# Optimization experiments

Measured on AMD Instinct MI355X. Metric: run time of the kernel, lower is better.

The kernel has to match this reference:

```python
import jax, jax.numpy as jnp
import numpy as np

B, H, W = 8, 64, 64
DIM, DIM_OUT, HEADS = 448, 896, 16
WIN, STRIDE = 14, 2
MLP_DIM = int(DIM_OUT * 4.0)
EPS = 1e-6
HD = DIM_OUT // HEADS
SCALE = HD ** -0.5


def _ln(x, g, b):
    m = jnp.mean(x, -1, keepdims=True)
    v = jnp.var(x, -1, keepdims=True)
    return (x - m) * jax.lax.rsqrt(v + EPS) * g + b


def _maxpool(x, s):
    # Keras MaxPool2D(pool_size=s, strides=s, padding='valid'), NHWC
    return jax.lax.reduce_window(x, -jnp.inf, jax.lax.max, (1, s, s, 1), (1, s, s, 1), 'VALID')


def setup_inputs() -> dict:
    key = jax.random.key(0)
    ks = jax.random.split(key, 8)
    rn = lambda k, shape: (jax.random.normal(k, shape, jnp.float32) * 0.02)
    return {
        "x": jax.random.normal(ks[0], (B, H, W, DIM), jnp.float32),
        "ln1_g": jnp.ones((DIM,), jnp.float32), "ln1_b": jnp.zeros((DIM,), jnp.float32),
        "qkv_w": rn(ks[1], (DIM, 3 * DIM_OUT)), "qkv_b": jnp.zeros((3 * DIM_OUT,), jnp.float32),
        "attn_proj_w": rn(ks[2], (DIM_OUT, DIM_OUT)), "attn_proj_b": jnp.zeros((DIM_OUT,), jnp.float32),
        "skip_w": rn(ks[3], (DIM, DIM_OUT)), "skip_b": jnp.zeros((DIM_OUT,), jnp.float32),
        "ln2_g": jnp.ones((DIM_OUT,), jnp.float32), "ln2_b": jnp.zeros((DIM_OUT,), jnp.float32),
        "mlp1_w": rn(ks[4], (DIM_OUT, MLP_DIM)), "mlp1_b": jnp.zeros((MLP_DIM,), jnp.float32),
        "mlp2_w": rn(ks[5], (MLP_DIM, DIM_OUT)), "mlp2_b": jnp.zeros((DIM_OUT,), jnp.float32),
    }


def reference(x, ln1_g, ln1_b, qkv_w, qkv_b, attn_proj_w, attn_proj_b,
              skip_w, skip_b, ln2_g, ln2_b, mlp1_w, mlp1_b, mlp2_w, mlp2_b):
    hn = _ln(x, ln1_g, ln1_b)                              # [B,H,W,DIM]
    # dim != dim_out: residual = proj(layernormed); then residual max-pooled
    shortcut = _maxpool(hn @ skip_w + skip_b, STRIDE)      # [B,H/2,W/2,DIM_OUT]

    # window partition (pad 64 -> 70, 5x5 windows of 14x14)
    pad_h = (WIN - H % WIN) % WIN
    pad_w = (WIN - W % WIN) % WIN
    hp = jnp.pad(hn, ((0, 0), (0, pad_h), (0, pad_w), (0, 0)))
    Hp, Wp = H + pad_h, W + pad_w
    nh, nw = Hp // WIN, Wp // WIN
    win = hp.reshape(B, nh, WIN, nw, WIN, DIM).transpose(0, 1, 3, 2, 4, 5)
    win = win.reshape(B * nh * nw, WIN, WIN, DIM)          # [Bw,14,14,DIM]

    # multi-scale attention with query pooling
    Bw = B * nh * nw
    qkv = (win @ qkv_w + qkv_b).reshape(Bw, WIN * WIN, 3, HEADS, HD)
    q, k, v = qkv[:, :, 0], qkv[:, :, 1], qkv[:, :, 2]
    q = _maxpool(q.reshape(Bw, WIN, WIN, DIM_OUT), STRIDE)  # [Bw,7,7,DIM_OUT]
    WQ = WIN // STRIDE
    q = q.reshape(Bw, WQ * WQ, HEADS, HD)
    attn = jax.nn.softmax(jnp.einsum('bqhd,bkhd->bhqk', q * SCALE, k), axis=-1)
    out = jnp.einsum('bhqk,bkhd->bqhd', attn, v).reshape(Bw, WQ, WQ, DIM_OUT)
    out = out @ attn_proj_w + attn_proj_b                  # [Bw,7,7,DIM_OUT]

    # window unpartition at pooled resolution (window 7, padded 35 -> crop 32)
    H2, W2 = H // STRIDE, W // STRIDE
    win2 = WIN // STRIDE
    Hp2 = H2 + (win2 - H2 % win2) % win2
    Wp2 = W2 + (win2 - W2 % win2) % win2
    xo = out.reshape(B, nh, nw, win2, win2, DIM_OUT).transpose(0, 1, 3, 2, 4, 5)
    xo = xo.reshape(B, Hp2, Wp2, DIM_OUT)[:, :H2, :W2, :]

    y = shortcut + xo
    hn2 = _ln(y, ln2_g, ln2_b)
    mlp = jax.nn.gelu(hn2 @ mlp1_w + mlp1_b, approximate=False) @ mlp2_w + mlp2_b
    return y + mlp
```

## Files before the change

### kernel.cpp

```cpp
#include <hip/hip_runtime.h>
#include <hip/hip_bf16.h>

typedef unsigned short u16;
typedef __bf16 bf16x8 __attribute__((ext_vector_type(8)));
typedef float f32x4 __attribute__((ext_vector_type(4)));

__device__ __forceinline__ float bf2f(u16 u) {
    unsigned v = ((unsigned)u) << 16;
    return __builtin_bit_cast(float, v);
}
__device__ __forceinline__ u16 f2bf(float f) {
    unsigned x = __builtin_bit_cast(unsigned, f);
    unsigned r = x + (0x7fffu + ((x >> 16) & 1u));
    return (u16)(r >> 16);
}
__device__ __forceinline__ void gload16(const void* g, void* l) {
    __builtin_amdgcn_global_load_lds(
        (const __attribute__((address_space(1))) void*)g,
        (__attribute__((address_space(3))) void*)l, 16, 0, 0);
}

__global__ __launch_bounds__(256) void transpose_w(const float* __restrict__ src,
    u16* __restrict__ dst, int K, int N)
{
    __shared__ u16 T[64][33];
    int k0 = blockIdx.x * 32, n0 = blockIdx.y * 64;
    int t = threadIdx.x;
    int nc = t & 63, krb = (t >> 6) * 8;
#pragma unroll
    for (int j = 0; j < 8; j++) {
        int kr = krb + j;
        T[nc][kr] = f2bf(src[(size_t)(k0 + kr) * N + n0 + nc]);
    }
    __syncthreads();
    int r = t >> 2, c0 = (t & 3) * 8;
    u16 tmp[8];
#pragma unroll
    for (int i = 0; i < 8; i++) tmp[i] = T[r][c0 + i];
    *(uint4*)&dst[(size_t)(n0 + r) * K + k0 + c0] = *(uint4*)tmp;
}

__global__ void zfill(u16* p) { p[threadIdx.x] = 0; }

template<int C>
__global__ __launch_bounds__(256) void ln_kernel(const float* __restrict__ xf,
    const float* __restrict__ g, const float* __restrict__ b,
    u16* __restrict__ out, int npix)
{
    int wid = threadIdx.x >> 6, lane = threadIdx.x & 63;
    int pix = blockIdx.x * 4 + wid;
    if (pix >= npix) return;
    constexpr int J = C / 64;
    float v[J];
    float s = 0.f, s2 = 0.f;
#pragma unroll
    for (int j = 0; j < J; j++) {
        int c = lane + j * 64;
        float t = xf[(size_t)pix * C + c];
        v[j] = t; s += t; s2 += t * t;
    }
#pragma unroll
    for (int off = 32; off; off >>= 1) {
        s  += __shfl_xor(s,  off, 64);
        s2 += __shfl_xor(s2, off, 64);
    }
    float mean = s / C;
    float var = fmaxf(s2 / C - mean * mean, 0.f);
    float rs = rsqrtf(var + 1e-6f);
#pragma unroll
    for (int j = 0; j < J; j++) {
        int c = lane + j * 64;
        float o = (v[j] - mean) * rs * g[c] + b[c];
        out[(size_t)pix * C + c] = f2bf(o);
    }
}

enum { GA_NONE = 0, GA_WIN = 1 };
enum { EPI_STORE = 0, EPI_GELU = 1, EPI_PROJ = 2, EPI_OUT = 3, EPI_QKV = 4,
       EPI_POOL = 5 };

template<int BM, int GATHER, int EPI, int SWZ>
__global__ __launch_bounds__(256, (BM == 64) ? 6 : 4) void gemm_t(
    const u16* __restrict__ A, const u16* __restrict__ BT,
    const u16* __restrict__ zrow, const float* __restrict__ bias,
    u16* __restrict__ Cb, u16* __restrict__ Cb2,
    float* __restrict__ Yf, float* __restrict__ Of,
    int M, int N, int K, int nbn)
{
    constexpr int MI = BM / 32;
    constexpr int PA = BM / 64;
    constexpr int ASZ = BM * 32, BSZ = 128 * 32;
    __shared__ __align__(16) u16 As[2][ASZ];
    __shared__ __align__(16) u16 Bs[2][BSZ];
    __shared__ int rowsrc[BM];

    const int tid = threadIdx.x;
    int bm, bn;
    if (SWZ) {
        int nwg = gridDim.x, orig = blockIdx.x;
        int q = nwg >> 3, r = nwg & 7;
        int xcd = orig & 7, idx = orig >> 3;
        int wg = (xcd < r ? xcd * (q + 1) : r * (q + 1) + (xcd - r) * q) + idx;
        bm = wg / nbn; bn = wg - bm * nbn;
    } else {
        bm = blockIdx.x; bn = blockIdx.y;
    }

    if (GATHER == GA_WIN) {
        if (tid < BM) {
            int gm = bm * BM + tid;
            int src = -1;
            if (gm < M) {
                int w = gm / 196, t = gm % 196;
                int b = w / 25, wh = (w / 5) % 5, ww = w % 5;
                int ty = t / 14, tx = t % 14;
                int gh = wh * 14 + ty, gw = ww * 14 + tx;
                if (gh < 64 && gw < 64) src = (b * 64 + gh) * 64 + gw;
            }
            rowsrc[tid] = src;
        }
        __syncthreads();
    }

    const int wid = tid >> 6, lane = tid & 63;
    const int wm = wid >> 1, wn = wid & 1;
    const int frow = lane & 15, quad = lane >> 4;

    const int srow = tid >> 2, schunk = tid & 3;
    const int ssw = schunk ^ ((srow ^ (srow >> 2)) & 3);

    const u16* gA[PA]; int stA[PA];
#pragma unroll
    for (int p = 0; p < PA; p++) {
        int r = srow + p * 64;
        int src;
        if (GATHER == GA_WIN) {
            src = rowsrc[r];
        } else {
            int gm = bm * BM + r;
            src = (gm < M) ? gm : -1;
        }
        gA[p]  = (src >= 0) ? A + (size_t)src * K + ssw * 8 : zrow + ssw * 8;
        stA[p] = (src >= 0) ? 32 : 0;
    }
    const u16* gB[2];
#pragma unroll
    for (int p = 0; p < 2; p++)
        gB[p] = BT + (size_t)(bn * 128 + srow + p * 64) * K + ssw * 8;

    const int csw = quad ^ ((frow ^ (frow >> 2)) & 3);
    int offA[MI], offB[4];
#pragma unroll
    for (int mi = 0; mi < MI; mi++)
        offA[mi] = (wm * (BM / 2) + mi * 16 + frow) * 32 + csw * 8;
#pragma unroll
    for (int ni = 0; ni < 4; ni++)
        offB[ni] = (wn * 64 + ni * 16 + frow) * 32 + csw * 8;

    f32x4 acc[MI][4] = {};

    auto stageAdv = [&](int buf) {
#pragma unroll
        for (int p = 0; p < PA; p++) {
            gload16(gA[p], &As[buf][tid * 8 + p * 2048]);
            gA[p] += stA[p];
        }
#pragma unroll
        for (int p = 0; p < 2; p++) {
            gload16(gB[p], &Bs[buf][tid * 8 + p * 2048]);
            gB[p] += 32;
        }
    };
    auto wait_loads = [&]() {
        if constexpr (PA == 2) asm volatile("s_waitcnt vmcnt(4)" ::: "memory");
        else                   asm volatile("s_waitcnt vmcnt(3)" ::: "memory");
    };

    stageAdv(0);
    stageAdv(1);
    wait_loads();
    __builtin_amdgcn_s_barrier();

    int cur = 0;
    const int NK = K / 32;
    for (int kt = 0; kt < NK; kt++) {
        bf16x8 af[MI], bfr[4];
#pragma unroll
        for (int mi = 0; mi < MI; mi++)
            af[mi] = *(const bf16x8*)&As[cur][offA[mi]];
#pragma unroll
        for (int ni = 0; ni < 4; ni++)
            bfr[ni] = *(const bf16x8*)&Bs[cur][offB[ni]];
        asm volatile("s_waitcnt lgkmcnt(0)" ::: "memory");
        __builtin_amdgcn_s_barrier();
        if (kt + 2 < NK) stageAdv(cur);

#pragma unroll
        for (int mi = 0; mi < MI; mi++)
#pragma unroll
            for (int ni = 0; ni < 4; ni++)
                acc[mi][ni] = __builtin_amdgcn_mfma_f32_16x16x32_bf16(
                    af[mi], bfr[ni], acc[mi][ni], 0, 0, 0);

        if (kt + 1 < NK) {
            if (kt + 2 < NK) wait_loads();
            else asm volatile("s_waitcnt vmcnt(0)" ::: "memory");
            __builtin_amdgcn_s_barrier();
        }
        cur ^= 1;
    }

    if (EPI == EPI_POOL) {
        __syncthreads();
        float* Pool = (float*)As;
        if (wm == 1) {
#pragma unroll
            for (int mi = 0; mi < MI; mi++)
#pragma unroll
            for (int ni = 0; ni < 4; ni++) {
                int ox0 = mi * 8 + quad * 2;
                int gnl = wn * 64 + ni * 16 + frow;
                Pool[(ox0 + 0) * 128 + gnl] = fmaxf(acc[mi][ni][0], acc[mi][ni][1]);
                Pool[(ox0 + 1) * 128 + gnl] = fmaxf(acc[mi][ni][2], acc[mi][ni][3]);
            }
        }
        __syncthreads();
        if (wm == 0) {
            int b = bm >> 5, oy = bm & 31;
#pragma unroll
            for (int mi = 0; mi < MI; mi++)
#pragma unroll
            for (int ni = 0; ni < 4; ni++) {
                int ox0 = mi * 8 + quad * 2;
                int gnl = wn * 64 + ni * 16 + frow;
                int gn = bn * 128 + gnl;
                float bv = bias[gn];
                float v0 = fmaxf(fmaxf(acc[mi][ni][0], acc[mi][ni][1]),
                                 Pool[(ox0 + 0) * 128 + gnl]) + bv;
                float v1 = fmaxf(fmaxf(acc[mi][ni][2], acc[mi][ni][3]),
                                 Pool[(ox0 + 1) * 128 + gnl]) + bv;
                size_t pix = (size_t)((b * 32 + oy) * 32 + ox0);
                Yf[pix * 896 + gn] = v0;
                Yf[(pix + 1) * 896 + gn] = v1;
            }
        }
        return;
    }

#pragma unroll
    for (int mi = 0; mi < MI; mi++)
#pragma unroll
    for (int ni = 0; ni < 4; ni++)
#pragma unroll
    for (int i = 0; i < 4; i++) {
        int gm = bm * BM + wm * (BM / 2) + mi * 16 + quad * 4 + i;
        int gn = bn * 128 + wn * 64 + ni * 16 + frow;
        if (gm >= M) continue;
        float val = acc[mi][ni][i] + bias[gn];
        if (EPI == EPI_STORE) {
            Cb[(size_t)gm * N + gn] = f2bf(val);
        } else if (EPI == EPI_QKV) {
            int third = gn / 896;
            int col = gn - third * 896;
            u16* dst = third ? Cb2 : Cb;
            dst[(size_t)gm * 896 + col] = f2bf(val);
        } else if (EPI == EPI_GELU) {
            float ge = 0.5f * val * (1.0f + erff(val * 0.70710678118654752f));
            Cb[(size_t)gm * N + gn] = f2bf(ge);
        } else if (EPI == EPI_PROJ) {
            int w = gm / 49, q = gm % 49;
            int b = w / 25, wh = (w / 5) % 5, ww = w % 5;
            int qy = q / 7, qx = q % 7;
            int oy = wh * 7 + qy, ox = ww * 7 + qx;
            if (oy < 32 && ox < 32) {
                size_t pix = (size_t)((b * 32 + oy) * 32 + ox);
                Yf[pix * 896 + gn] += val;
            }
        } else {
            Of[(size_t)gm * 896 + gn] = val + Yf[(size_t)gm * 896 + gn];
        }
    }
}

__global__ __launch_bounds__(256) void qpool(const u16* __restrict__ qf,
                                             u16* __restrict__ qp, int total8)
{
    int id = blockIdx.x * 256 + threadIdx.x;
    if (id >= total8) return;
    int c8 = id % 112, rq = id / 112;
    int c = c8 * 8;
    int q = rq % 49, w = rq / 49;
    int qy = q / 7, qx = q % 7;
    int t0 = (2 * qy) * 14 + 2 * qx;
    const u16* base = qf + (size_t)(w * 196 + t0) * 896 + c;
    uint4 a = *(const uint4*)base;
    uint4 b = *(const uint4*)(base + 896);
    uint4 cc = *(const uint4*)(base + 14 * 896);
    uint4 d = *(const uint4*)(base + 15 * 896);
    u16 ua[8], ub[8], uc[8], ud[8], uo[8];
    *(uint4*)ua = a; *(uint4*)ub = b; *(uint4*)uc = cc; *(uint4*)ud = d;
#pragma unroll
    for (int i = 0; i < 8; i++) {
        float m = fmaxf(fmaxf(bf2f(ua[i]), bf2f(ub[i])),
                        fmaxf(bf2f(uc[i]), bf2f(ud[i])));
        uo[i] = f2bf(m);
    }
    *(uint4*)&qp[(size_t)rq * 896 + c] = *(uint4*)uo;
}

__global__ __launch_bounds__(256) void attn_mfma(const u16* __restrict__ qp,
    const u16* __restrict__ kbuf, const u16* __restrict__ vbuf,
    u16* __restrict__ ao)
{
    __shared__ __align__(16) u16 Ps[64][232];
    __shared__ __align__(16) u16 KV[208 * 72];

    const float SCALE = 0.13363062095621219f;
    const int w = blockIdx.x >> 4, h = blockIdx.x & 15;
    const int tid = threadIdx.x;
    const int wid = tid >> 6, lane = tid & 63;
    const int n16 = lane & 15, quad = lane >> 4;

    for (int idx = tid; idx < 64 * 232 / 8; idx += 256)
        *(uint4*)&Ps[0][idx * 8] = make_uint4(0u, 0u, 0u, 0u);
    for (int idx = tid; idx < 208 * 9; idx += 256) {
        int n = idx / 9, kc = (idx % 9) * 8;
        uint4 val = make_uint4(0u, 0u, 0u, 0u);
        if (n < 196 && kc < 56)
            val = *(const uint4*)(kbuf + (size_t)(w * 196 + n) * 896 + h * 56 + kc);
        *(uint4*)&KV[n * 72 + kc] = val;
    }
    bf16x8 qf[2];
    {
        int m = 16 * wid + n16;
        int row = w * 49 + (m < 49 ? m : 48);
        const u16* src = qp + (size_t)row * 896 + h * 56;
#pragma unroll
        for (int ks = 0; ks < 2; ks++) {
            int kk = ks * 32 + quad * 8;
            uint4 v = make_uint4(0u, 0u, 0u, 0u);
            if (kk < 56) v = *(const uint4*)(src + kk);
            qf[ks] = __builtin_bit_cast(bf16x8, v);
        }
    }
    __syncthreads();

    f32x4 S[13] = {};
#pragma unroll
    for (int nt = 0; nt < 13; nt++) {
#pragma unroll
        for (int ks = 0; ks < 2; ks++) {
            bf16x8 bf = *(const bf16x8*)&KV[(nt * 16 + n16) * 72 + ks * 32 + quad * 8];
            S[nt] = __builtin_amdgcn_mfma_f32_16x16x32_bf16(qf[ks], bf, S[nt], 0, 0, 0);
        }
    }
#pragma unroll
    for (int i = 0; i < 4; i++) {
        float mx = -3.0e38f;
#pragma unroll
        for (int nt = 0; nt < 13; nt++) {
            float v = S[nt][i] * SCALE;
            S[nt][i] = v;
            if (nt < 12 || n16 < 4) mx = fmaxf(mx, v);
        }
        mx = fmaxf(mx, __shfl_xor(mx, 1, 64));
        mx = fmaxf(mx, __shfl_xor(mx, 2, 64));
        mx = fmaxf(mx, __shfl_xor(mx, 4, 64));
        mx = fmaxf(mx, __shfl_xor(mx, 8, 64));
        float sm = 0.f;
#pragma unroll
        for (int nt = 0; nt < 13; nt++) {
            float e = (nt < 12 || n16 < 4) ? __expf(S[nt][i] - mx) : 0.f;
            S[nt][i] = e;
            sm += e;
        }
        sm += __shfl_xor(sm, 1, 64);
        sm += __shfl_xor(sm, 2, 64);
        sm += __shfl_xor(sm, 4, 64);
        sm += __shfl_xor(sm, 8, 64);
        float inv = 1.f / sm;
#pragma unroll
        for (int nt = 0; nt < 13; nt++) S[nt][i] *= inv;
    }
    __syncthreads();

#pragma unroll
    for (int nt = 0; nt < 13; nt++)
#pragma unroll
        for (int i = 0; i < 4; i++)
            Ps[16 * wid + 4 * quad + i][16 * nt + n16] = f2bf(S[nt][i]);

    u16 (*Vs)[232] = reinterpret_cast<u16(*)[232]>(KV);
    for (int idx = tid; idx < 98 * 7; idx += 256) {
        int j2 = idx / 7, dc = idx % 7;
        int j = 2 * j2;
        const u16* vp = vbuf + (size_t)(w * 196 + j) * 896 + h * 56 + dc * 8;
        uint4 a = *(const uint4*)vp;
        uint4 b = *(const uint4*)(vp + 896);
        u16 ua[8], ub[8];
        *(uint4*)ua = a; *(uint4*)ub = b;
#pragma unroll
        for (int i = 0; i < 8; i++) {
            unsigned pair = (unsigned)ua[i] | ((unsigned)ub[i] << 16);
            *(unsigned*)&Vs[dc * 8 + i][j] = pair;
        }
    }
    for (int idx = tid; idx < 64 * 14; idx += 256) {
        int d = idx / 14, c = idx % 14;
        *(unsigned*)&Vs[d][196 + 2 * c] = 0u;
    }
    __syncthreads();

    f32x4 O[4] = {};
#pragma unroll
    for (int ks = 0; ks < 7; ks++) {
        bf16x8 a = *(const bf16x8*)&Ps[16 * wid + n16][ks * 32 + quad * 8];
#pragma unroll
        for (int nt = 0; nt < 4; nt++) {
            bf16x8 b = *(const bf16x8*)&Vs[16 * nt + n16][ks * 32 + quad * 8];
            O[nt] = __builtin_amdgcn_mfma_f32_16x16x32_bf16(a, b, O[nt], 0, 0, 0);
        }
    }
#pragma unroll
    for (int nt = 0; nt < 4; nt++)
#pragma unroll
        for (int i = 0; i < 4; i++) {
            int m = 16 * wid + 4 * quad + i;
            int d = 16 * nt + n16;
            if (m < 49 && d < 56)
                ao[(size_t)(w * 49 + m) * 896 + h * 56 + d] = f2bf(O[nt][i]);
        }
}

extern "C" void kernel_launch(void* const* d_in, const int* in_sizes, int n_in,
                              void* d_out, int out_size, void* d_ws, size_t ws_size,
                              hipStream_t stream)
{
    const float* x    = (const float*)d_in[0];
    const float* ln1g = (const float*)d_in[1];
    const float* ln1b = (const float*)d_in[2];
    const float* qkvw = (const float*)d_in[3];
    const float* qkvb = (const float*)d_in[4];
    const float* pw   = (const float*)d_in[5];
    const float* pb   = (const float*)d_in[6];
    const float* sw   = (const float*)d_in[7];
    const float* sb   = (const float*)d_in[8];
    const float* ln2g = (const float*)d_in[9];
    const float* ln2b = (const float*)d_in[10];
    const float* m1w  = (const float*)d_in[11];
    const float* m1b  = (const float*)d_in[12];
    const float* m2w  = (const float*)d_in[13];
    const float* m2b  = (const float*)d_in[14];

    char* ws = (char*)d_ws;
    u16*   slot1 = (u16*)(ws + 0);
    u16*   vbuf  = (u16*)(ws + 70246400);
    u16*   hn    = (u16*)(ws + 140492800);
    float* Yf    = (float*)(ws + 169852928);
    u16*   qp    = (u16*)(ws + 199213056);
    u16*   ao    = (u16*)(ws + 216774656);
    u16*   swT   = (u16*)(ws + 234336256);
    u16*   qkvT  = (u16*)(ws + 235139072);
    u16*   pwT   = (u16*)(ws + 237547520);
    u16*   zrow  = (u16*)(ws + 239153152);
    u16*   qfull = slot1;
    u16*   kbuf  = slot1;
    u16*   m1    = slot1;
    u16*   hn2   = hn;
    u16*   m1wT  = vbuf;
    u16*   m2wT  = (u16*)(ws + 70246400 + 6422528);
    float* outf  = (float*)d_out;

    zfill<<<1, 128, 0, stream>>>(zrow);
    transpose_w<<<dim3(14, 14), 256, 0, stream>>>(sw,   swT,  448, 896);
    transpose_w<<<dim3(14, 42), 256, 0, stream>>>(qkvw, qkvT, 448, 2688);
    transpose_w<<<dim3(28, 14), 256, 0, stream>>>(pw,   pwT,  896, 896);
    ln_kernel<448><<<8192, 256, 0, stream>>>(x, ln1g, ln1b, hn, 32768);
    gemm_t<128, GA_NONE, EPI_POOL, 1><<<256 * 7, 256, 0, stream>>>(
        hn, swT, zrow, sb, nullptr, nullptr, Yf, nullptr, 32768, 896, 448, 7);
    gemm_t<128, GA_WIN, EPI_STORE, 1><<<307 * 7, 256, 0, stream>>>(
        hn, qkvT, zrow, qkvb, qfull, nullptr, nullptr, nullptr, 39200, 896, 448, 7);
    qpool<<<4288, 256, 0, stream>>>(qfull, qp, 9800 * 112);
    gemm_t<128, GA_WIN, EPI_QKV, 1><<<307 * 14, 256, 0, stream>>>(
        hn, qkvT + (size_t)896 * 448, zrow, qkvb + 896, kbuf, vbuf, nullptr, nullptr,
        39200, 1792, 448, 14);
    attn_mfma<<<3200, 256, 0, stream>>>(qp, kbuf, vbuf, ao);
    transpose_w<<<dim3(28, 56),  256, 0, stream>>>(m1w, m1wT, 896, 3584);
    transpose_w<<<dim3(112, 14), 256, 0, stream>>>(m2w, m2wT, 3584, 896);
    gemm_t<64, GA_NONE, EPI_PROJ, 1><<<154 * 7, 256, 0, stream>>>(
        ao, pwT, zrow, pb, nullptr, nullptr, Yf, nullptr, 9800, 896, 896, 7);
    ln_kernel<896><<<2048, 256, 0, stream>>>(Yf, ln2g, ln2b, hn2, 8192);
    gemm_t<128, GA_NONE, EPI_GELU, 0><<<dim3(64, 28), 256, 0, stream>>>(
        hn2, m1wT, zrow, m1b, m1, nullptr, nullptr, nullptr, 8192, 3584, 896, 28);
    gemm_t<64, GA_NONE, EPI_OUT, 0><<<dim3(128, 7), 256, 0, stream>>>(
        m1, m2wT, zrow, m2b, nullptr, nullptr, Yf, outf, 8192, 896, 3584, 7);
}
```

Measured before the change: 699.1 us.

## Compute QKV on unpadded image and fuse query max-pool into GEMM epilogue

The windowed QKV GEMMs with gather over padded 39200 rows are replaced by one GEMM over the 32768 real pixels producing K and V in image layout, with Q max-pooled in the epilogue and scattered to window order. Padded positions are served by the bias (converted to bf16) in the attention loader and by a separate fill kernel for pooled Q. This removes padded-row compute, the full-resolution Q write/read, and the separate qpool kernel. In exchange attention loads gain per-element address arithmetic and branching.

```diff
diff --git a/kernel.cpp b/kernel.cpp
--- a/kernel.cpp
+++ b/kernel.cpp
@@ -41,6 +41,30 @@
 }
 
 __global__ void zfill(u16* p) { p[threadIdx.x] = 0; }
+
+__global__ __launch_bounds__(256) void cvt_bias(const float* __restrict__ s,
+                                                u16* __restrict__ d, int n)
+{
+    int i = blockIdx.x * 256 + threadIdx.x;
+    if (i < n) d[i] = f2bf(s[i]);
+}
+
+__global__ __launch_bounds__(256) void qfill(const float* __restrict__ qkvb,
+                                             u16* __restrict__ qp)
+{
+    int id = blockIdx.x * 256 + threadIdx.x;
+    if (id >= 9800 * 112) return;
+    int c8 = id % 112, rq = id / 112;
+    int q = rq % 49, w = rq / 49;
+    int qy = q / 7, qx = q - 7 * qy;
+    int wh = (w / 5) % 5, ww = w % 5;
+    if (!((wh == 4 && qy >= 4) || (ww == 4 && qx >= 4))) return;
+    int c = c8 * 8;
+    u16 o[8];
+#pragma unroll
+    for (int i = 0; i < 8; i++) o[i] = f2bf(qkvb[c + i]);
+    *(uint4*)&qp[(size_t)rq * 896 + c] = *(uint4*)o;
+}
 
 template<int C>
 __global__ __launch_bounds__(256) void ln_kernel(const float* __restrict__ xf,
@@ -75,15 +99,14 @@
     }
 }
 
-enum { GA_NONE = 0, GA_WIN = 1 };
-enum { EPI_STORE = 0, EPI_GELU = 1, EPI_PROJ = 2, EPI_OUT = 3, EPI_QKV = 4,
+enum { EPI_STORE = 0, EPI_GELU = 1, EPI_PROJ = 2, EPI_OUT = 3, EPI_QKV3 = 4,
        EPI_POOL = 5 };
 
-template<int BM, int GATHER, int EPI, int SWZ>
+template<int BM, int EPI, int SWZ>
 __global__ __launch_bounds__(256, (BM == 64) ? 6 : 4) void gemm_t(
     const u16* __restrict__ A, const u16* __restrict__ BT,
     const u16* __restrict__ zrow, const float* __restrict__ bias,
-    u16* __restrict__ Cb, u16* __restrict__ Cb2,
+    u16* __restrict__ Cb, u16* __restrict__ Cb2, u16* __restrict__ Cb3,
     float* __restrict__ Yf, float* __restrict__ Of,
     int M, int N, int K, int nbn)
 {
@@ -92,7 +115,6 @@
     constexpr int ASZ = BM * 32, BSZ = 128 * 32;
     __shared__ __align__(16) u16 As[2][ASZ];
     __shared__ __align__(16) u16 Bs[2][BSZ];
-    __shared__ int rowsrc[BM];
 
     const int tid = threadIdx.x;
     int bm, bn;
@@ -106,22 +128,6 @@
         bm = blockIdx.x; bn = blockIdx.y;
     }
 
-    if (GATHER == GA_WIN) {
-        if (tid < BM) {
-            int gm = bm * BM + tid;
-            int src = -1;
-            if (gm < M) {
-                int w = gm / 196, t = gm % 196;
-                int b = w / 25, wh = (w / 5) % 5, ww = w % 5;
-                int ty = t / 14, tx = t % 14;
-                int gh = wh * 14 + ty, gw = ww * 14 + tx;
-                if (gh < 64 && gw < 64) src = (b * 64 + gh) * 64 + gw;
-            }
-            rowsrc[tid] = src;
-        }
-        __syncthreads();
-    }
-
     const int wid = tid >> 6, lane = tid & 63;
     const int wm = wid >> 1, wn = wid & 1;
     const int frow = lane & 15, quad = lane >> 4;
@@ -132,14 +138,8 @@
     const u16* gA[PA]; int stA[PA];
 #pragma unroll
     for (int p = 0; p < PA; p++) {
-        int r = srow + p * 64;
-        int src;
-        if (GATHER == GA_WIN) {
-            src = rowsrc[r];
-        } else {
-            int gm = bm * BM + r;
-            src = (gm < M) ? gm : -1;
-        }
+        int gm = bm * BM + srow + p * 64;
+        int src = (gm < M) ? gm : -1;
         gA[p]  = (src >= 0) ? A + (size_t)src * K + ssw * 8 : zrow + ssw * 8;
         stA[p] = (src >= 0) ? 32 : 0;
     }
@@ -210,7 +210,8 @@
         cur ^= 1;
     }
 
-    if (EPI == EPI_POOL) {
+    const bool qpool_path = (EPI == EPI_QKV3 && bn < 7) || EPI == EPI_POOL;
+    if (qpool_path) {
         __syncthreads();
         float* Pool = (float*)As;
         if (wm == 1) {
@@ -227,6 +228,7 @@
         __syncthreads();
         if (wm == 0) {
             int b = bm >> 5, oy = bm & 31;
+            int wh = oy / 7, qy = oy - 7 * wh;
 #pragma unroll
             for (int mi = 0; mi < MI; mi++)
 #pragma unroll
@@ -239,9 +241,19 @@
                                  Pool[(ox0 + 0) * 128 + gnl]) + bv;
                 float v1 = fmaxf(fmaxf(acc[mi][ni][2], acc[mi][ni][3]),
                                  Pool[(ox0 + 1) * 128 + gnl]) + bv;
-                size_t pix = (size_t)((b * 32 + oy) * 32 + ox0);
-                Yf[pix * 896 + gn] = v0;
-                Yf[(pix + 1) * 896 + gn] = v1;
+                if (EPI == EPI_POOL) {
+                    size_t pix = (size_t)((b * 32 + oy) * 32 + ox0);
+                    Yf[pix * 896 + gn] = v0;
+                    Yf[(pix + 1) * 896 + gn] = v1;
+                } else {
+                    int ox1 = ox0 + 1;
+                    int ww0 = ox0 / 7, qx0 = ox0 - 7 * ww0;
+                    int ww1 = ox1 / 7, qx1 = ox1 - 7 * ww1;
+                    int w0 = b * 25 + wh * 5 + ww0;
+                    int w1 = b * 25 + wh * 5 + ww1;
+                    Cb3[(size_t)(w0 * 49 + qy * 7 + qx0) * 896 + gn] = f2bf(v0);
+                    Cb3[(size_t)(w1 * 49 + qy * 7 + qx1) * 896 + gn] = f2bf(v1);
+                }
             }
         }
         return;
@@ -259,10 +271,10 @@
         float val = acc[mi][ni][i] + bias[gn];
         if (EPI == EPI_STORE) {
             Cb[(size_t)gm * N + gn] = f2bf(val);
-        } else if (EPI == EPI_QKV) {
+        } else if (EPI == EPI_QKV3) {
             int third = gn / 896;
             int col = gn - third * 896;
-            u16* dst = third ? Cb2 : Cb;
+            u16* dst = (third == 1) ? Cb : Cb2;
             dst[(size_t)gm * 896 + col] = f2bf(val);
         } else if (EPI == EPI_GELU) {
             float ge = 0.5f * val * (1.0f + erff(val * 0.70710678118654752f));
@@ -282,35 +294,9 @@
     }
 }
 
-__global__ __launch_bounds__(256) void qpool(const u16* __restrict__ qf,
-                                             u16* __restrict__ qp, int total8)
-{
-    int id = blockIdx.x * 256 + threadIdx.x;
-    if (id >= total8) return;
-    int c8 = id % 112, rq = id / 112;
-    int c = c8 * 8;
-    int q = rq % 49, w = rq / 49;
-    int qy = q / 7, qx = q % 7;
-    int t0 = (2 * qy) * 14 + 2 * qx;
-    const u16* base = qf + (size_t)(w * 196 + t0) * 896 + c;
-    uint4 a = *(const uint4*)base;
-    uint4 b = *(const uint4*)(base + 896);
-    uint4 cc = *(const uint4*)(base + 14 * 896);
-    uint4 d = *(const uint4*)(base + 15 * 896);
-    u16 ua[8], ub[8], uc[8], ud[8], uo[8];
-    *(uint4*)ua = a; *(uint4*)ub = b; *(uint4*)uc = cc; *(uint4*)ud = d;
-#pragma unroll
-    for (int i = 0; i < 8; i++) {
-        float m = fmaxf(fmaxf(bf2f(ua[i]), bf2f(ub[i])),
-                        fmaxf(bf2f(uc[i]), bf2f(ud[i])));
-        uo[i] = f2bf(m);
-    }
-    *(uint4*)&qp[(size_t)rq * 896 + c] = *(uint4*)uo;
-}
-
 __global__ __launch_bounds__(256) void attn_mfma(const u16* __restrict__ qp,
-    const u16* __restrict__ kbuf, const u16* __restrict__ vbuf,
-    u16* __restrict__ ao)
+    const u16* __restrict__ kimg, const u16* __restrict__ vimg,
+    const u16* __restrict__ qkvbf, u16* __restrict__ ao)
 {
     __shared__ __align__(16) u16 Ps[64][232];
     __shared__ __align__(16) u16 KV[208 * 72];
@@ -321,13 +307,22 @@
     const int wid = tid >> 6, lane = tid & 63;
     const int n16 = lane & 15, quad = lane >> 4;
 
+    const int b = w / 25, wh = (w / 5) % 5, ww = w % 5;
+    const int ghb = wh * 14, gwb = ww * 14;
+
     for (int idx = tid; idx < 64 * 232 / 8; idx += 256)
         *(uint4*)&Ps[0][idx * 8] = make_uint4(0u, 0u, 0u, 0u);
     for (int idx = tid; idx < 208 * 9; idx += 256) {
         int n = idx / 9, kc = (idx % 9) * 8;
         uint4 val = make_uint4(0u, 0u, 0u, 0u);
-        if (n < 196 && kc < 56)
-            val = *(const uint4*)(kbuf + (size_t)(w * 196 + n) * 896 + h * 56 + kc);
+        if (n < 196 && kc < 56) {
+            int ty = n / 14, tx = n - 14 * ty;
+            int gh = ghb + ty, gw = gwb + tx;
+            const u16* src = (gh < 64 && gw < 64)
+                ? kimg + (size_t)((b * 64 + gh) * 64 + gw) * 896 + h * 56 + kc
+                : qkvbf + 896 + h * 56 + kc;
+            val = *(const uint4*)src;
+        }
         *(uint4*)&KV[n * 72 + kc] = val;
     }
     bf16x8 qf[2];
@@ -394,11 +389,19 @@
     for (int idx = tid; idx < 98 * 7; idx += 256) {
         int j2 = idx / 7, dc = idx % 7;
         int j = 2 * j2;
-        const u16* vp = vbuf + (size_t)(w * 196 + j) * 896 + h * 56 + dc * 8;
-        uint4 a = *(const uint4*)vp;
-        uint4 b = *(const uint4*)(vp + 896);
+        int ty = j / 14, tx = j - 14 * ty;
+        int gh = ghb + ty, gw = gwb + tx;
+        int off = h * 56 + dc * 8;
+        const u16* p0 = (gh < 64 && gw < 64)
+            ? vimg + (size_t)((b * 64 + gh) * 64 + gw) * 896 + off
+            : qkvbf + 1792 + off;
+        const u16* p1 = (gh < 64 && gw + 1 < 64)
+            ? vimg + (size_t)((b * 64 + gh) * 64 + gw + 1) * 896 + off
+            : qkvbf + 1792 + off;
+        uint4 a = *(const uint4*)p0;
+        uint4 bb = *(const uint4*)p1;
         u16 ua[8], ub[8];
-        *(uint4*)ua = a; *(uint4*)ub = b;
+        *(uint4*)ua = a; *(uint4*)ub = bb;
 #pragma unroll
         for (int i = 0; i < 8; i++) {
             unsigned pair = (unsigned)ua[i] | ((unsigned)ub[i] << 16);
@@ -417,8 +420,8 @@
         bf16x8 a = *(const bf16x8*)&Ps[16 * wid + n16][ks * 32 + quad * 8];
 #pragma unroll
         for (int nt = 0; nt < 4; nt++) {
-            bf16x8 b = *(const bf16x8*)&Vs[16 * nt + n16][ks * 32 + quad * 8];
-            O[nt] = __builtin_amdgcn_mfma_f32_16x16x32_bf16(a, b, O[nt], 0, 0, 0);
+            bf16x8 b2 = *(const bf16x8*)&Vs[16 * nt + n16][ks * 32 + quad * 8];
+            O[nt] = __builtin_amdgcn_mfma_f32_16x16x32_bf16(a, b2, O[nt], 0, 0, 0);
         }
     }
 #pragma unroll
@@ -453,45 +456,47 @@
     const float* m2b  = (const float*)d_in[14];
 
     char* ws = (char*)d_ws;
-    u16*   slot1 = (u16*)(ws + 0);
-    u16*   vbuf  = (u16*)(ws + 70246400);
-    u16*   hn    = (u16*)(ws + 140492800);
-    float* Yf    = (float*)(ws + 169852928);
-    u16*   qp    = (u16*)(ws + 199213056);
-    u16*   ao    = (u16*)(ws + 216774656);
-    u16*   swT   = (u16*)(ws + 234336256);
-    u16*   qkvT  = (u16*)(ws + 235139072);
-    u16*   pwT   = (u16*)(ws + 237547520);
-    u16*   zrow  = (u16*)(ws + 239153152);
-    u16*   qfull = slot1;
-    u16*   kbuf  = slot1;
-    u16*   m1    = slot1;
-    u16*   hn2   = hn;
-    u16*   m1wT  = vbuf;
-    u16*   m2wT  = (u16*)(ws + 70246400 + 6422528);
-    float* outf  = (float*)d_out;
+    u16*   kimg = (u16*)(ws + 0);
+    u16*   vimg = (u16*)(ws + 58720256);
+    u16*   hn   = (u16*)(ws + 117440512);
+    float* Yf   = (float*)(ws + 146800640);
+    u16*   qp   = (u16*)(ws + 176160768);
+    u16*   ao   = (u16*)(ws + 193722368);
+    u16*   swT  = (u16*)(ws + 211283968);
+    u16*   qkvT = (u16*)(ws + 212086784);
+    u16*   pwT  = (u16*)(ws + 214495232);
+    u16*   qkvbf= (u16*)(ws + 216100864);
+    u16*   zrow = (u16*)(ws + 216106240);
+    u16*   m1   = kimg;
+    u16*   hn2  = hn;
+    u16*   m1wT = vimg;
+    u16*   m2wT = (u16*)(ws + 58720256 + 6422528);
+    float* outf = (float*)d_out;
 
     zfill<<<1, 128, 0, stream>>>(zrow);
+    cvt_bias<<<11, 256, 0, stream>>>(qkvb, qkvbf, 2688);
+    qfill<<<4288, 256, 0, stream>>>(qkvb, qp);
     transpose_w<<<dim3(14, 14), 256, 0, stream>>>(sw,   swT,  448, 896);
     transpose_w<<<dim3(14, 42), 256, 0, stream>>>(qkvw, qkvT, 448, 2688);
     transpose_w<<<dim3(28, 14), 256, 0, stream>>>(pw,   pwT,  896, 896);
     ln_kernel<448><<<8192, 256, 0, stream>>>(x, ln1g, ln1b, hn, 32768);
-    gemm_t<128, GA_NONE, EPI_POOL, 1><<<256 * 7, 256, 0, stream>>>(
-        hn, swT, zrow, sb, nullptr, nullptr, Yf, nullptr, 32768, 896, 448, 7);
-    gemm_t<128, GA_WIN, EPI_STORE, 1><<<307 * 7, 256, 0, stream>>>(
-        hn, qkvT, zrow, qkvb, qfull, nullptr, nullptr, nullptr, 39200, 896, 448, 7);
-    qpool<<<4288, 256, 0, stream>>>(qfull, qp, 9800 * 112);
-    gemm_t<128, GA_WIN, EPI_QKV, 1><<<307 * 14, 256, 0, stream>>>(
-        hn, qkvT + (size_t)896 * 448, zrow, qkvb + 896, kbuf, vbuf, nullptr, nullptr,
-        39200, 1792, 448, 14);
-    attn_mfma<<<3200, 256, 0, stream>>>(qp, kbuf, vbuf, ao);
+    gemm_t<128, EPI_POOL, 1><<<256 * 7, 256, 0, stream>>>(
+        hn, swT, zrow, sb, nullptr, nullptr, nullptr, Yf, nullptr,
+        32768, 896, 448, 7);
+    gemm_t<128, EPI_QKV3, 1><<<256 * 21, 256, 0, stream>>>(
+        hn, qkvT, zrow, qkvb, kimg, vimg, qp, nullptr, nullptr,
+        32768, 2688, 448, 21);
+    attn_mfma<<<3200, 256, 0, stream>>>(qp, kimg, vimg, qkvbf, ao);
     transpose_w<<<dim3(28, 56),  256, 0, stream>>>(m1w, m1wT, 896, 3584);
     transpose_w<<<dim3(112, 14), 256, 0, stream>>>(m2w, m2wT, 3584, 896);
-    gemm_t<64, GA_NONE, EPI_PROJ, 1><<<154 * 7, 256, 0, stream>>>(
-        ao, pwT, zrow, pb, nullptr, nullptr, Yf, nullptr, 9800, 896, 896, 7);
+    gemm_t<64, EPI_PROJ, 1><<<154 * 7, 256, 0, stream>>>(
+        ao, pwT, zrow, pb, nullptr, nullptr, nullptr, Yf, nullptr,
+        9800, 896, 896, 7);
     ln_kernel<896><<<2048, 256, 0, stream>>>(Yf, ln2g, ln2b, hn2, 8192);
-    gemm_t<128, GA_NONE, EPI_GELU, 0><<<dim3(64, 28), 256, 0, stream>>>(
-        hn2, m1wT, zrow, m1b, m1, nullptr, nullptr, nullptr, 8192, 3584, 896, 28);
-    gemm_t<64, GA_NONE, EPI_OUT, 0><<<dim3(128, 7), 256, 0, stream>>>(
-        m1, m2wT, zrow, m2b, nullptr, nullptr, Yf, outf, 8192, 896, 3584, 7);
-}
+    gemm_t<128, EPI_GELU, 0><<<dim3(64, 28), 256, 0, stream>>>(
+        hn2, m1wT, zrow, m1b, m1, nullptr, nullptr, nullptr, nullptr,
+        8192, 3584, 896, 28);
+    gemm_t<64, EPI_OUT, 0><<<dim3(128, 7), 256, 0, stream>>>(
+        m1, m2wT, zrow, m2b, nullptr, nullptr, nullptr, Yf, outf,
+        8192, 896, 3584, 7);
+}
```

After: 621.7 us. 11.1% less time.
